# Kernel tuning notes

Measured on AMD Instinct MI355X. Metric: run time of the kernel, lower is better.

## Reference

```python
import jax, jax.numpy as jnp
import numpy as np

B, T, D = 4, 2048, 512
E, H, K = 8, 512, 2


def setup_inputs() -> dict:
    key = jax.random.key(0)
    ks = jax.random.split(key, 8)
    s_in = 1.0 / np.sqrt(D)
    s_h = 1.0 / np.sqrt(H)
    return {
        "x": jax.random.normal(ks[0], (B, T, D), dtype=jnp.float32),
        "Wg": jax.random.uniform(ks[1], (D, E), jnp.float32, -s_in, s_in),
        "bg": jax.random.uniform(ks[2], (E,), jnp.float32, -s_in, s_in),
        "W1": jax.random.uniform(ks[3], (E, D, H), jnp.float32, -s_in, s_in),
        "b1": jax.random.uniform(ks[4], (E, H), jnp.float32, -s_in, s_in),
        "W2": jax.random.uniform(ks[5], (E, H, H), jnp.float32, -s_h, s_h),
        "b2": jax.random.uniform(ks[6], (E, H), jnp.float32, -s_h, s_h),
    }


def reference(x, Wg, bg, W1, b1, W2, b2):
    Bx, Tx, Dx = x.shape
    xf = x.reshape(-1, Dx)                                   # [N, D]
    # --- gate (noise_std = 0) ---
    logits = xf @ Wg + bg                                    # [N, E]
    topk_scores, topk_idx = jax.lax.top_k(logits, K)         # [N, K]
    topk_w = jax.nn.softmax(topk_scores, axis=-1)            # K=2 -> softmax over selected
    # --- experts: dense compute, then gather the selected ones ---
    h = jax.nn.gelu(jnp.einsum('nd,edh->neh', xf, W1) + b1, approximate=False)  # [N, E, H]
    y = jnp.einsum('neh,ehf->nef', h, W2) + b2               # [N, E, H]
    sel = jnp.take_along_axis(y, topk_idx[:, :, None], axis=1)  # [N, K, H]
    out = jnp.sum(topk_w[:, :, None] * sel, axis=1)          # weighted combine [N, H]
    return out.reshape(Bx, Tx, -1)
```

## Files before the change

### kernel.cpp

```cpp
#include <hip/hip_runtime.h>
#include <hip/hip_bf16.h>


typedef __bf16 bf16x8 __attribute__((ext_vector_type(8)));
typedef float  f32x4  __attribute__((ext_vector_type(4)));

#define N_TOK 8192
#define D_IN  512
#define N_EXP 8
#define H_DIM 512

static __device__ __forceinline__ unsigned short f2bf(float f) {
    union { float f; unsigned u; } v; v.f = f;
    unsigned r = v.u + 0x7FFFu + ((v.u >> 16) & 1u);
    return (unsigned short)(r >> 16);
}
static __device__ __forceinline__ float bf2f(unsigned short h) {
    union { unsigned u; float f; } v; v.u = ((unsigned)h) << 16; return v.f;
}
static __device__ __forceinline__ float gelu_exact(float v) {
    return 0.5f * v * (1.0f + erff(v * 0.70710678118654752f));
}

__global__ void __launch_bounds__(256) k_pack(const float* __restrict__ W1,
                                              const float* __restrict__ W2,
                                              unsigned short* __restrict__ w1f,
                                              unsigned short* __restrict__ w2f) {
    __shared__ float t[32][65];
    int z = blockIdx.z;
    int e = z & 7;
    const float* in = (z < 8) ? W1 : W2;
    unsigned short* out = (z < 8) ? w1f : w2f;
    int cb0 = blockIdx.x * 4;
    int kc  = blockIdx.y;
    const float* src = in + ((size_t)e * 512 + kc * 32) * 512 + blockIdx.x * 64;
    int tid = threadIdx.x;
    int r = tid >> 3, cq = (tid & 7) * 8;
    float4 v0 = *(const float4*)(src + (size_t)r * 512 + cq);
    float4 v1 = *(const float4*)(src + (size_t)r * 512 + cq + 4);
    t[r][cq + 0] = v0.x; t[r][cq + 1] = v0.y; t[r][cq + 2] = v0.z; t[r][cq + 3] = v0.w;
    t[r][cq + 4] = v1.x; t[r][cq + 5] = v1.y; t[r][cq + 6] = v1.z; t[r][cq + 7] = v1.w;
    __syncthreads();
    int g = tid >> 6, lane = tid & 63;
    int l15 = lane & 15, l4 = lane >> 4;
    unsigned v[4];
    #pragma unroll
    for (int j = 0; j < 4; ++j) {
        unsigned lo = f2bf(t[l4 * 8 + 2 * j    ][g * 16 + l15]);
        unsigned hi = f2bf(t[l4 * 8 + 2 * j + 1][g * 16 + l15]);
        v[j] = lo | (hi << 16);
    }
    size_t dst = (((size_t)(e * 32 + cb0 + g) * 16 + kc) * 512) + lane * 8;
    *(uint4*)(out + dst) = make_uint4(v[0], v[1], v[2], v[3]);
}

__global__ void __launch_bounds__(256) k_gate(const float* __restrict__ x,
                                              const float* __restrict__ Wg,
                                              const float* __restrict__ bg,
                                              unsigned char* __restrict__ sel,
                                              float2* __restrict__ w2) {
    __shared__ float part[32][8][8];
    __shared__ float lg[32][8];
    int tid = threadIdx.x;
    int t = tid >> 3, c = tid & 7;
    int n = blockIdx.x * 32 + t;
    const float4* xr = (const float4*)(x + (size_t)n * D_IN + c * 64);
    float acc[8];
    #pragma unroll
    for (int e = 0; e < 8; ++e) acc[e] = 0.f;
    #pragma unroll
    for (int j4 = 0; j4 < 16; ++j4) {
        float4 v = xr[j4];
        int k = c * 64 + j4 * 4;
        float xv[4] = {v.x, v.y, v.z, v.w};
        #pragma unroll
        for (int u = 0; u < 4; ++u) {
            float4 wlo = *(const float4*)(Wg + (size_t)(k + u) * 8);
            float4 whi = *(const float4*)(Wg + (size_t)(k + u) * 8 + 4);
            acc[0] += xv[u] * wlo.x; acc[1] += xv[u] * wlo.y;
            acc[2] += xv[u] * wlo.z; acc[3] += xv[u] * wlo.w;
            acc[4] += xv[u] * whi.x; acc[5] += xv[u] * whi.y;
            acc[6] += xv[u] * whi.z; acc[7] += xv[u] * whi.w;
        }
    }
    #pragma unroll
    for (int e = 0; e < 8; ++e) part[t][c][e] = acc[e];
    __syncthreads();
    {
        float f = bg[c];
        #pragma unroll
        for (int cc = 0; cc < 8; ++cc) f += part[t][cc][c];
        lg[t][c] = f;
    }
    __syncthreads();
    if (c == 0) {
        float best = lg[t][0]; int i1 = 0;
        #pragma unroll
        for (int j = 1; j < 8; ++j) { float v = lg[t][j]; if (v > best) { best = v; i1 = j; } }
        float best2 = -1e30f; int i2 = 0;
        #pragma unroll
        for (int j = 0; j < 8; ++j) {
            if (j == i1) continue;
            float v = lg[t][j]; if (v > best2) { best2 = v; i2 = j; }
        }
        float tt = expf(best2 - best);
        float w0 = 1.0f / (1.0f + tt);
        sel[n] = (unsigned char)(i1 | (i2 << 4));
        w2[n] = make_float2(w0, 1.0f - w0);
    }
}

__global__ void __launch_bounds__(1024) k_build(const unsigned char* __restrict__ sel,
                                                const float2* __restrict__ w2,
                                                int* __restrict__ counts,
                                                int* __restrict__ lists,
                                                float* __restrict__ wgts) {
    int e = blockIdx.x;
    __shared__ int wave_tot[16], wave_base[16];
    int tid = threadIdx.x;
    int lane = tid & 63, wv = tid >> 6;
    int base = 0;
    for (int c0 = 0; c0 < N_TOK; c0 += 1024) {
        int n = c0 + tid;
        unsigned char s = sel[n];
        bool f1 = ((s & 15) == e);
        bool f = f1 || ((s >> 4) == e);
        unsigned long long mask = __ballot(f);
        int prefix = __popcll(mask & ((1ull << lane) - 1ull));
        if (lane == 0) wave_tot[wv] = __popcll(mask);
        __syncthreads();
        if (tid < 16) {
            int wb = 0;
            for (int i = 0; i < tid; ++i) wb += wave_tot[i];
            wave_base[tid] = wb;
        }
        __syncthreads();
        if (f) {
            int pos = base + wave_base[wv] + prefix;
            lists[e * N_TOK + pos] = (n << 1) | (f1 ? 0 : 1);
            float2 w = w2[n];
            wgts[e * N_TOK + pos] = f1 ? w.x : w.y;
        }
        base += wave_base[15] + wave_tot[15];
        __syncthreads();
    }
    if (tid == 0) counts[e] = base;
}

__global__ void __launch_bounds__(512, 4)
k_l1(const float* __restrict__ x,
     const unsigned short* __restrict__ w1f, const float* __restrict__ b1,
     const int* __restrict__ counts, const int* __restrict__ lists,
     unsigned short* __restrict__ hbuf) {
    __shared__ unsigned short lds[64 * D_IN];
    __shared__ int tl[64];

    int b = blockIdx.x;
    int e = b & 7;
    int rest = b >> 3;
    int tile = rest >> 1, ch = rest & 1;
    int cnt = counts[e];
    int row0 = tile * 64;
    if (row0 >= cnt) return;
    int rv = min(64, cnt - row0);
    int gb = row0;
    #pragma unroll
    for (int i = 0; i < 8; ++i) gb += (i < e) ? ((counts[i] + 63) & ~63) : 0;

    int tid = threadIdx.x, lane = tid & 63, wid = tid >> 6;
    int l15 = lane & 15, l4 = lane >> 4;
    if (tid < 64) tl[tid] = (tid < rv) ? lists[e * N_TOK + row0 + tid] : 0;

    const unsigned short* wbase = w1f + ((size_t)(e * 32 + ch * 16 + wid * 2) * 16) * 512 + (size_t)lane * 8;
    bf16x8 bb[3][2];
    #pragma unroll
    for (int n = 0; n < 2; ++n) {
        bb[0][n] = *(const bf16x8*)(wbase + (n * 16 + 0) * 512);
        bb[1][n] = *(const bf16x8*)(wbase + (n * 16 + 1) * 512);
    }
    float bv[2];
    #pragma unroll
    for (int n = 0; n < 2; ++n) bv[n] = b1[e * H_DIM + ch * 256 + wid * 32 + n * 16 + l15];
    __syncthreads();

    #pragma unroll
    for (int it = 0; it < 16; ++it) {
        int idx = tid + it * 512;
        int r = idx >> 7, c4 = idx & 127;
        float4 v = make_float4(0.f, 0.f, 0.f, 0.f);
        if (r < rv)
            v = ((const float4*)(x + (size_t)(tl[r] >> 1) * D_IN))[c4];
        unsigned lo = (unsigned)f2bf(v.x) | ((unsigned)f2bf(v.y) << 16);
        unsigned hi = (unsigned)f2bf(v.z) | ((unsigned)f2bf(v.w) << 16);
        int off = (r * 1024 + c4 * 8) ^ ((r & 7) << 4);
        *(uint2*)((char*)lds + off) = make_uint2(lo, hi);
    }
    __syncthreads();

    f32x4 acc[4][2];
    #pragma unroll
    for (int n = 0; n < 2; ++n)
        #pragma unroll
        for (int m = 0; m < 4; ++m) acc[m][n] = f32x4{bv[n], bv[n], bv[n], bv[n]};

    #pragma unroll
    for (int kc = 0; kc < 16; ++kc) {
        if (kc + 2 < 16) {
            #pragma unroll
            for (int n = 0; n < 2; ++n)
                bb[(kc + 2) % 3][n] = *(const bf16x8*)(wbase + (n * 16 + kc + 2) * 512);
        }
        int k0 = kc * 32 + l4 * 8;
        bf16x8 a[4];
        #pragma unroll
        for (int m = 0; m < 4; ++m) {
            int row = m * 16 + l15;
            int off = (row * 1024 + k0 * 2) ^ ((row & 7) << 4);
            a[m] = *(const bf16x8*)((const char*)lds + off);
        }
        #pragma unroll
        for (int n = 0; n < 2; ++n)
            #pragma unroll
            for (int m = 0; m < 4; ++m)
                acc[m][n] = __builtin_amdgcn_mfma_f32_16x16x32_bf16(a[m], bb[kc % 3][n], acc[m][n], 0, 0, 0);
    }
    __syncthreads();

    #pragma unroll
    for (int m = 0; m < 4; ++m)
        #pragma unroll
        for (int n = 0; n < 2; ++n)
            #pragma unroll
            for (int r = 0; r < 4; ++r) {
                int row = m * 16 + l4 * 4 + r;
                int lcol = wid * 32 + n * 16 + l15;
                lds[row * 256 + lcol] = f2bf(gelu_exact(acc[m][n][r]));
            }
    __syncthreads();
    #pragma unroll
    for (int it = 0; it < 4; ++it) {
        int idx = tid + it * 512;
        int row = idx >> 5, g = idx & 31;
        if (row < rv)
            *(uint4*)(hbuf + (size_t)(gb + row) * 512 + ch * 256 + g * 8) =
                *(uint4*)(lds + row * 256 + g * 8);
    }
}

template <bool SLOT>
__global__ void __launch_bounds__(512, 4)
k_l2(const unsigned short* __restrict__ hbuf,
     const unsigned short* __restrict__ w2f, const float* __restrict__ b2,
     const int* __restrict__ counts, const int* __restrict__ lists,
     const float* __restrict__ wgts,
     unsigned short* __restrict__ ybuf, float* __restrict__ out) {
    __shared__ unsigned short lds[64 * D_IN];
    __shared__ int   tl[64];
    __shared__ float wl[64];

    int b = blockIdx.x;
    int e = b & 7;
    int rest = b >> 3;
    int tile = rest >> 1, ch = rest & 1;
    int cnt = counts[e];
    int row0 = tile * 64;
    if (row0 >= cnt) return;
    int rv = min(64, cnt - row0);
    int gb = row0;
    #pragma unroll
    for (int i = 0; i < 8; ++i) gb += (i < e) ? ((counts[i] + 63) & ~63) : 0;

    int tid = threadIdx.x, lane = tid & 63, wid = tid >> 6;
    int l15 = lane & 15, l4 = lane >> 4;
    if (tid < 64) {
        int v = 0; float w = 0.f;
        if (tid < rv) {
            v = lists[e * N_TOK + row0 + tid];
            w = wgts [e * N_TOK + row0 + tid];
        }
        tl[tid] = v; wl[tid] = w;
    }

    const unsigned short* wbase = w2f + ((size_t)(e * 32 + ch * 16 + wid * 2) * 16) * 512 + (size_t)lane * 8;
    bf16x8 bb[3][2];
    #pragma unroll
    for (int n = 0; n < 2; ++n) {
        bb[0][n] = *(const bf16x8*)(wbase + (n * 16 + 0) * 512);
        bb[1][n] = *(const bf16x8*)(wbase + (n * 16 + 1) * 512);
    }
    float bv[2];
    #pragma unroll
    for (int n = 0; n < 2; ++n) bv[n] = b2[e * H_DIM + ch * 256 + wid * 32 + n * 16 + l15];
    __syncthreads();

    #pragma unroll
    for (int it = 0; it < 8; ++it) {
        int idx = tid + it * 512;
        int r = idx >> 6, g = idx & 63;
        uint4 v = make_uint4(0, 0, 0, 0);
        if (r < rv)
            v = *(const uint4*)(hbuf + (size_t)(gb + r) * 512 + g * 8);
        int off = (r * 1024 + g * 16) ^ ((r & 7) << 4);
        *(uint4*)((char*)lds + off) = v;
    }
    __syncthreads();

    f32x4 acc[4][2];
    #pragma unroll
    for (int n = 0; n < 2; ++n)
        #pragma unroll
        for (int m = 0; m < 4; ++m) acc[m][n] = f32x4{bv[n], bv[n], bv[n], bv[n]};

    #pragma unroll
    for (int kc = 0; kc < 16; ++kc) {
        if (kc + 2 < 16) {
            #pragma unroll
            for (int n = 0; n < 2; ++n)
                bb[(kc + 2) % 3][n] = *(const bf16x8*)(wbase + (n * 16 + kc + 2) * 512);
        }
        int k0 = kc * 32 + l4 * 8;
        bf16x8 a[4];
        #pragma unroll
        for (int m = 0; m < 4; ++m) {
            int row = m * 16 + l15;
            int off = (row * 1024 + k0 * 2) ^ ((row & 7) << 4);
            a[m] = *(const bf16x8*)((const char*)lds + off);
        }
        #pragma unroll
        for (int n = 0; n < 2; ++n)
            #pragma unroll
            for (int m = 0; m < 4; ++m)
                acc[m][n] = __builtin_amdgcn_mfma_f32_16x16x32_bf16(a[m], bb[kc % 3][n], acc[m][n], 0, 0, 0);
    }

    if (SLOT) {
        __syncthreads();
        #pragma unroll
        for (int m = 0; m < 4; ++m)
            #pragma unroll
            for (int n = 0; n < 2; ++n)
                #pragma unroll
                for (int r = 0; r < 4; ++r) {
                    int row = m * 16 + l4 * 4 + r;
                    int lcol = wid * 32 + n * 16 + l15;
                    lds[row * 256 + lcol] = f2bf(acc[m][n][r] * wl[row]);
                }
        __syncthreads();
        #pragma unroll
        for (int it = 0; it < 4; ++it) {
            int idx = tid + it * 512;
            int row = idx >> 5, g = idx & 31;
            if (row < rv)
                *(uint4*)(ybuf + (size_t)tl[row] * 512 + ch * 256 + g * 8) =
                    *(uint4*)(lds + row * 256 + g * 8);
        }
    } else {
        #pragma unroll
        for (int m = 0; m < 4; ++m)
            #pragma unroll
            for (int r = 0; r < 4; ++r) {
                int row = m * 16 + l4 * 4 + r;
                if (row < rv) {
                    int t = tl[row] >> 1;
                    float gw = wl[row];
                    #pragma unroll
                    for (int n = 0; n < 2; ++n) {
                        int col = ch * 256 + wid * 32 + n * 16 + l15;
                        atomicAdd(out + (size_t)t * H_DIM + col, gw * acc[m][n][r]);
                    }
                }
            }
    }
}

__global__ void __launch_bounds__(256) k_combine(const unsigned short* __restrict__ yb,
                                                 float* __restrict__ out) {
    int gid = blockIdx.x * 256 + threadIdx.x;
    int n = gid >> 6;
    int h0 = (gid & 63) * 8;
    const unsigned short* r0 = yb + ((size_t)2 * n) * H_DIM + h0;
    uint4 a = *(const uint4*)r0;
    uint4 b = *(const uint4*)(r0 + H_DIM);
    float o[8];
    unsigned ua[4] = {a.x, a.y, a.z, a.w}, ub[4] = {b.x, b.y, b.z, b.w};
    #pragma unroll
    for (int j = 0; j < 4; ++j) {
        o[2 * j]     = bf2f((unsigned short)(ua[j] & 0xFFFF)) + bf2f((unsigned short)(ub[j] & 0xFFFF));
        o[2 * j + 1] = bf2f((unsigned short)(ua[j] >> 16))    + bf2f((unsigned short)(ub[j] >> 16));
    }
    float* dst = out + (size_t)n * H_DIM + h0;
    *(float4*)dst       = make_float4(o[0], o[1], o[2], o[3]);
    *(float4*)(dst + 4) = make_float4(o[4], o[5], o[6], o[7]);
}

extern "C" void kernel_launch(void* const* d_in, const int* in_sizes, int n_in,
                              void* d_out, int out_size, void* d_ws, size_t ws_size,
                              hipStream_t stream) {
    (void)in_sizes; (void)n_in;
    const float* x  = (const float*)d_in[0];
    const float* Wg = (const float*)d_in[1];
    const float* bg = (const float*)d_in[2];
    const float* W1 = (const float*)d_in[3];
    const float* b1 = (const float*)d_in[4];
    const float* W2 = (const float*)d_in[5];
    const float* b2 = (const float*)d_in[6];
    float* out = (float*)d_out;

    char* ws = (char*)d_ws;
    const size_t tail_sz = 256 + 262144 + 262144 + 8192 + 65536;
    size_t need1 = (41ull << 20) + tail_sz;
    size_t need2 = (25ull << 20) + tail_sz;

    unsigned short* w1f = (unsigned short*)(ws);
    unsigned short* w2f = (unsigned short*)(ws + (4ull << 20));
    unsigned short* ybuf = nullptr;
    unsigned short* hbuf = nullptr;
    char* tail;
    int mode;
    if (ws_size >= need1) {
        mode = 0;
        ybuf = (unsigned short*)(ws + (8ull << 20));
        hbuf = (unsigned short*)(ws + (24ull << 20));
        tail = ws + (41ull << 20);
    } else if (ws_size >= need2) {
        mode = 1;
        hbuf = (unsigned short*)(ws + (8ull << 20));
        tail = ws + (25ull << 20);
    } else {
        mode = 1;
        hbuf = (unsigned short*)(ws + (8ull << 20));
        tail = ws + (25ull << 20);
    }
    int*   counts = (int*)(tail);
    int*   lists  = (int*)(tail + 256);
    float* wgts   = (float*)(tail + 256 + 262144);
    unsigned char* sel = (unsigned char*)(tail + 256 + 524288);
    float2* w2g   = (float2*)(tail + 256 + 532480);

    if (mode == 1)
        hipMemsetAsync(out, 0, (size_t)out_size * sizeof(float), stream);

    k_pack<<<dim3(8, 16, 16), dim3(256), 0, stream>>>(W1, W2, w1f, w2f);
    k_gate<<<dim3(N_TOK / 32), dim3(256), 0, stream>>>(x, Wg, bg, sel, w2g);
    k_build<<<dim3(N_EXP), dim3(1024), 0, stream>>>(sel, w2g, counts, lists, wgts);
    k_l1<<<dim3(2048), dim3(512), 0, stream>>>(x, w1f, b1, counts, lists, hbuf);
    if (mode == 0) {
        k_l2<true><<<dim3(2048), dim3(512), 0, stream>>>(
            hbuf, w2f, b2, counts, lists, wgts, ybuf, out);
        k_combine<<<dim3(N_TOK * 64 / 256), dim3(256), 0, stream>>>(ybuf, out);
    } else {
        k_l2<false><<<dim3(2048), dim3(512), 0, stream>>>(
            hbuf, w2f, b2, counts, lists, wgts, hbuf , out);
    }
}
```

Measured before the change: 175.3 us.

## Pre-convert x to bf16 in gate kernel and stage tiles via global_load_lds

The gate kernel now also writes a bf16 copy of x. The first expert layer gathers rows from that copy instead of converting fp32 rows itself, which halves gather traffic and removes duplicate conversion, since each token is gathered by two experts. Both expert kernels now fill LDS with direct global-to-LDS loads, applying the XOR swizzle on the source address. This needs an extra 8 MB of workspace and an extra write of x, and it relies on the lane-ordered LDS write matching the swizzled layout.

```diff
diff --git a/kernel.cpp b/kernel.cpp
--- a/kernel.cpp
+++ b/kernel.cpp
@@ -20,6 +20,11 @@
 }
 static __device__ __forceinline__ float gelu_exact(float v) {
     return 0.5f * v * (1.0f + erff(v * 0.70710678118654752f));
+}
+static __device__ __forceinline__ void gload_lds16(const void* src, void* lds_dst) {
+    __builtin_amdgcn_global_load_lds(
+        (const __attribute__((address_space(1))) unsigned int*)src,
+        (__attribute__((address_space(3))) unsigned int*)lds_dst, 16, 0, 0);
 }
 
 __global__ void __launch_bounds__(256) k_pack(const float* __restrict__ W1,
@@ -58,12 +63,14 @@
                                               const float* __restrict__ Wg,
                                               const float* __restrict__ bg,
                                               unsigned char* __restrict__ sel,
-                                              float2* __restrict__ w2) {
+                                              float2* __restrict__ w2,
+                                              unsigned short* __restrict__ xbf) {
     __shared__ float part[32][8][8];
     __shared__ float lg[32][8];
     int tid = threadIdx.x;
     int t = tid >> 3, c = tid & 7;
-    int n = blockIdx.x * 32 + t;
+    int n0 = blockIdx.x * 32;
+    int n = n0 + t;
     const float4* xr = (const float4*)(x + (size_t)n * D_IN + c * 64);
     float acc[8];
     #pragma unroll
@@ -107,6 +114,19 @@
         float w0 = 1.0f / (1.0f + tt);
         sel[n] = (unsigned char)(i1 | (i2 << 4));
         w2[n] = make_float2(w0, 1.0f - w0);
+    }
+    #pragma unroll
+    for (int i = 0; i < 8; ++i) {
+        int idx = tid + i * 256;
+        int r = idx >> 6, g = idx & 63;
+        const float* src = x + (size_t)(n0 + r) * D_IN + g * 8;
+        float4 a = *(const float4*)src;
+        float4 b = *(const float4*)(src + 4);
+        unsigned u0 = (unsigned)f2bf(a.x) | ((unsigned)f2bf(a.y) << 16);
+        unsigned u1 = (unsigned)f2bf(a.z) | ((unsigned)f2bf(a.w) << 16);
+        unsigned u2 = (unsigned)f2bf(b.x) | ((unsigned)f2bf(b.y) << 16);
+        unsigned u3 = (unsigned)f2bf(b.z) | ((unsigned)f2bf(b.w) << 16);
+        *(uint4*)(xbf + (size_t)(n0 + r) * D_IN + g * 8) = make_uint4(u0, u1, u2, u3);
     }
 }
 
@@ -148,7 +168,7 @@
 }
 
 __global__ void __launch_bounds__(512, 4)
-k_l1(const float* __restrict__ x,
+k_l1(const unsigned short* __restrict__ xbf,
      const unsigned short* __restrict__ w1f, const float* __restrict__ b1,
      const int* __restrict__ counts, const int* __restrict__ lists,
      unsigned short* __restrict__ hbuf) {
@@ -184,16 +204,16 @@
     __syncthreads();
 
     #pragma unroll
-    for (int it = 0; it < 16; ++it) {
-        int idx = tid + it * 512;
-        int r = idx >> 7, c4 = idx & 127;
-        float4 v = make_float4(0.f, 0.f, 0.f, 0.f);
-        if (r < rv)
-            v = ((const float4*)(x + (size_t)(tl[r] >> 1) * D_IN))[c4];
-        unsigned lo = (unsigned)f2bf(v.x) | ((unsigned)f2bf(v.y) << 16);
-        unsigned hi = (unsigned)f2bf(v.z) | ((unsigned)f2bf(v.w) << 16);
-        int off = (r * 1024 + c4 * 8) ^ ((r & 7) << 4);
-        *(uint2*)((char*)lds + off) = make_uint2(lo, hi);
+    for (int i = 0; i < 8; ++i) {
+        int row = wid * 8 + i;
+        if (row < rv) {
+            int tok = tl[row] >> 1;
+            const char* src = (const char*)xbf + ((size_t)tok << 10)
+                            + ((lane * 16) ^ ((row & 7) << 4));
+            gload_lds16(src, (char*)lds + row * 1024);
+        } else {
+            *(uint4*)((char*)lds + row * 1024 + lane * 16) = make_uint4(0, 0, 0, 0);
+        }
     }
     __syncthreads();
 
@@ -294,14 +314,15 @@
     __syncthreads();
 
     #pragma unroll
-    for (int it = 0; it < 8; ++it) {
-        int idx = tid + it * 512;
-        int r = idx >> 6, g = idx & 63;
-        uint4 v = make_uint4(0, 0, 0, 0);
-        if (r < rv)
-            v = *(const uint4*)(hbuf + (size_t)(gb + r) * 512 + g * 8);
-        int off = (r * 1024 + g * 16) ^ ((r & 7) << 4);
-        *(uint4*)((char*)lds + off) = v;
+    for (int i = 0; i < 8; ++i) {
+        int row = wid * 8 + i;
+        if (row < rv) {
+            const char* src = (const char*)hbuf + (((size_t)(gb + row)) << 10)
+                            + ((lane * 16) ^ ((row & 7) << 4));
+            gload_lds16(src, (char*)lds + row * 1024);
+        } else {
+            *(uint4*)((char*)lds + row * 1024 + lane * 16) = make_uint4(0, 0, 0, 0);
+        }
     }
     __syncthreads();
 
@@ -408,28 +429,27 @@
 
     char* ws = (char*)d_ws;
     const size_t tail_sz = 256 + 262144 + 262144 + 8192 + 65536;
-    size_t need1 = (41ull << 20) + tail_sz;
-    size_t need2 = (25ull << 20) + tail_sz;
+    size_t need1 = (49ull << 20) + tail_sz;
+    size_t need2 = (33ull << 20) + tail_sz;
 
     unsigned short* w1f = (unsigned short*)(ws);
     unsigned short* w2f = (unsigned short*)(ws + (4ull << 20));
     unsigned short* ybuf = nullptr;
     unsigned short* hbuf = nullptr;
+    unsigned short* xbf  = nullptr;
     char* tail;
     int mode;
     if (ws_size >= need1) {
         mode = 0;
         ybuf = (unsigned short*)(ws + (8ull << 20));
         hbuf = (unsigned short*)(ws + (24ull << 20));
-        tail = ws + (41ull << 20);
-    } else if (ws_size >= need2) {
-        mode = 1;
-        hbuf = (unsigned short*)(ws + (8ull << 20));
-        tail = ws + (25ull << 20);
+        xbf  = (unsigned short*)(ws + (41ull << 20));
+        tail = ws + (49ull << 20);
     } else {
         mode = 1;
         hbuf = (unsigned short*)(ws + (8ull << 20));
-        tail = ws + (25ull << 20);
+        xbf  = (unsigned short*)(ws + (25ull << 20));
+        tail = ws + (33ull << 20);
     }
     int*   counts = (int*)(tail);
     int*   lists  = (int*)(tail + 256);
@@ -441,9 +461,9 @@
         hipMemsetAsync(out, 0, (size_t)out_size * sizeof(float), stream);
 
     k_pack<<<dim3(8, 16, 16), dim3(256), 0, stream>>>(W1, W2, w1f, w2f);
-    k_gate<<<dim3(N_TOK / 32), dim3(256), 0, stream>>>(x, Wg, bg, sel, w2g);
+    k_gate<<<dim3(N_TOK / 32), dim3(256), 0, stream>>>(x, Wg, bg, sel, w2g, xbf);
     k_build<<<dim3(N_EXP), dim3(1024), 0, stream>>>(sel, w2g, counts, lists, wgts);
-    k_l1<<<dim3(2048), dim3(512), 0, stream>>>(x, w1f, b1, counts, lists, hbuf);
+    k_l1<<<dim3(2048), dim3(512), 0, stream>>>(xbf, w1f, b1, counts, lists, hbuf);
     if (mode == 0) {
         k_l2<true><<<dim3(2048), dim3(512), 0, stream>>>(
             hbuf, w2f, b2, counts, lists, wgts, ybuf, out);
```

Measured after the change: 168.5 us. 3.9% less time.
